# Performance work log

Measured on AMD Instinct MI355X. Metric: run time of the kernel, lower is better.

Reference implementation:

```python
import jax, jax.numpy as jnp
import numpy as np

N = 50000      # nodes
E = 800000     # edges (avg degree 16)
NF = 128       # input feature dim
H = 128        # hidden dim
GAMMA = 1.0    # gm init arg
COS_EPS = 1e-8 # F.cosine_similarity eps
EW_MIN = 1e-4  # edge-weight clamp


def setup_inputs() -> dict:
    key = jax.random.key(0)
    ks = jax.random.split(key, 9)
    x = jax.random.normal(ks[0], (N, NF), dtype=jnp.float32)
    edge_index = jax.random.randint(ks[1], (2, E), 0, N, dtype=jnp.int64)
    sensitive_attr = jax.random.randint(ks[2], (N,), 0, 2, dtype=jnp.int64)
    s1 = 1.0 / np.sqrt(NF)
    s2 = 1.0 / np.sqrt(H)
    W1 = jax.random.normal(ks[3], (NF, H), dtype=jnp.float32) * s1
    b1 = jnp.zeros((H,), dtype=jnp.float32)
    W2 = jax.random.normal(ks[4], (H, H), dtype=jnp.float32) * s2
    b2 = jnp.zeros((H,), dtype=jnp.float32)
    Wc = jax.random.normal(ks[5], (H, 1), dtype=jnp.float32) * s2
    bc = jnp.zeros((1,), dtype=jnp.float32)
    return {"x": x, "edge_index": edge_index, "sensitive_attr": sensitive_attr,
            "W1": W1, "b1": b1, "W2": W2, "b2": b2, "Wc": Wc, "bc": bc}


def gcn_conv(x, W, b, src, dst, ew, n):
    """PyG GCNConv: lin -> symmetric-normalized edge-weighted aggregation (+self loops) -> bias."""
    xt = x @ W                                              # [N,H]
    deg = jax.ops.segment_sum(ew, dst, num_segments=n) + 1.0  # self-loop weight 1
    dinv = jnp.where(deg > 0, deg ** -0.5, 0.0)             # [N]
    norm = dinv[src] * ew * dinv[dst]                       # [E]
    agg = jax.ops.segment_sum(xt[src] * norm[:, None], dst, num_segments=n)
    # self-loop contribution: norm_ii = dinv[i] * 1 * dinv[i]
    return agg + xt * (dinv * dinv)[:, None] + b


def reference(x, edge_index, sensitive_attr, W1, b1, W2, b2, Wc, bc):
    src, dst = edge_index[0], edge_index[1]
    # cosine-similarity edge weights (gather-heavy)
    xs, xd = x[src], x[dst]                                  # [E,F] each
    dot = jnp.sum(xs * xd, axis=1)
    ns = jnp.maximum(jnp.sqrt(jnp.sum(xs * xs, axis=1)), COS_EPS)
    nd = jnp.maximum(jnp.sqrt(jnp.sum(xd * xd, axis=1)), COS_EPS)
    sim = dot / (ns * nd)
    sen_diff = (sensitive_attr[src] != sensitive_attr[dst]).astype(x.dtype)
    ew = jnp.maximum(sim * jnp.exp(-GAMMA * sen_diff), EW_MIN)
    # two GCN layers (dropout is identity in eval mode)
    h = jax.nn.relu(gcn_conv(x, W1, b1, src, dst, ew, N))
    h = jax.nn.relu(gcn_conv(h, W2, b2, src, dst, ew, N))
    y = h @ Wc + bc                                          # [N,1]
    return (y, h)
```

## Files before the change

kernel.cpp:

```cpp
#include <hip/hip_runtime.h>


typedef unsigned short u16;
typedef unsigned int u32;
typedef __attribute__((ext_vector_type(8))) short short8;
typedef __attribute__((ext_vector_type(4))) float floatx4;

__device__ __forceinline__ float bflo(u32 u){ return __uint_as_float(u << 16); }
__device__ __forceinline__ float bfhi(u32 u){ return __uint_as_float(u & 0xFFFF0000u); }
__device__ __forceinline__ float bf1(u16 u){ return __uint_as_float(((u32)u) << 16); }
__device__ __forceinline__ u16 f2bf(float f){
    u32 u = __float_as_uint(f);
    u += 0x7FFFu + ((u >> 16) & 1u);
    return (u16)(u >> 16);
}
__device__ __forceinline__ u32 pack2(float a, float b){
    return (u32)f2bf(a) | ((u32)f2bf(b) << 16);
}
__device__ __forceinline__ float wsum(float v){
#pragma unroll
    for (int o = 32; o > 0; o >>= 1) v += __shfl_xor(v, o, 64);
    return v;
}
__device__ __forceinline__ float ld1(const void* p, size_t idx, int f32){
    return f32 ? ((const float*)p)[idx] : bf1(((const u16*)p)[idx]);
}
__device__ __forceinline__ int ldidx(const int* p, size_t i, int i64){
    return i64 ? p[2 * i] : p[i];
}

__global__ void classify_k(const u32* __restrict__ xw, const int* __restrict__ eiw,
                           int* __restrict__ flags)
{
    __shared__ int c_out, c_nz;
    int t = threadIdx.x;
    if (t == 0) { c_out = 0; c_nz = 0; }
    __syncthreads();
    u32 w = xw[t];
    int e = (w >> 7) & 0xFF;
    int outl = (e < 110 || e > 140) ? 1 : 0;
    int nz = (eiw[2 * t + 1] != 0) ? 1 : 0;
    atomicAdd(&c_out, outl);
    atomicAdd(&c_nz, nz);
    __syncthreads();
    if (t == 0) { flags[0] = (c_out > 256); flags[1] = (c_nz < 256); }
}

__global__ __launch_bounds__(256) void convhist_k(const void* __restrict__ x,
                                                  u32* __restrict__ xb,
                                                  float* __restrict__ rn, int N,
                                                  const int* __restrict__ ei,
                                                  const int* __restrict__ sa,
                                                  int* __restrict__ cnt, int E,
                                                  const void* __restrict__ W1,
                                                  const void* __restrict__ W2,
                                                  uint4* __restrict__ wf1,
                                                  uint4* __restrict__ wf2,
                                                  const int* __restrict__ flags,
                                                  int nbN, int nbE)
{
    int b = blockIdx.x;
    if (b < nbN) {
        int i = b * 4 + (threadIdx.x >> 6);
        if (i >= N) return;
        int lane = threadIdx.x & 63;
        u32 u;
        if (flags[0]) {
            const float* q = (const float*)x + (size_t)i * 128 + lane * 2;
            u = pack2(q[0], q[1]);
        } else u = ((const u32*)x)[(size_t)i * 64 + lane];
        xb[(size_t)i * 64 + lane] = u;
        float f0 = bflo(u), f1 = bfhi(u);
        float ss = wsum(f0 * f0 + f1 * f1);
        if (lane == 0) {
            float r = 1.0f / fmaxf(sqrtf(ss), 1e-8f);
            int a = flags[1] ? sa[2 * (size_t)i] : sa[i];
            rn[i] = a ? -r : r;
        }
    } else if (b < nbN + nbE) {
        int e = (b - nbN) * 256 + threadIdx.x;
        if (e >= E) return;
        int d = ldidx(ei, (size_t)E + e, flags[1]);
        if ((u32)d >= (u32)N) d = 0;
        atomicAdd(&cnt[d], 1);
    } else {
        int slot = (b - nbN - nbE) * 256 + threadIdx.x;
        if (slot >= 4096) return;
        int f32w = flags[0];
        const void* W = (slot < 2048) ? W1 : W2;
        uint4* wf = (slot < 2048) ? wf1 : wf2;
        int s = slot & 2047;
        int lane = s & 63, kk = (s >> 6) & 3, ct = s >> 8;
        int q = lane >> 4, n = lane & 15;
        int col = ct * 16 + n, k0 = kk * 32 + q * 8;
        union { u16 us[8]; uint4 u4; } tmp;
#pragma unroll
        for (int j = 0; j < 8; ++j)
            tmp.us[j] = f2bf(ld1(W, (size_t)(k0 + j) * 128 + col, f32w));
        wf[s] = tmp.u4;
    }
}

__global__ __launch_bounds__(256) void scanA_k(int* __restrict__ cnt,
                                               int* __restrict__ rowp,
                                               int* __restrict__ bsum, int N)
{
    __shared__ int wtot[4];
    int t = threadIdx.x, lane = t & 63, w = t >> 6;
    int i0 = blockIdx.x * 1024 + t * 4;
    int v[4];
#pragma unroll
    for (int k = 0; k < 4; ++k) {
        int i = i0 + k;
        v[k] = (i < N) ? cnt[i] : 0;
        if (i < N) cnt[i] = 0;
    }
    int t4 = v[0] + v[1] + v[2] + v[3];
    int sc = t4;
#pragma unroll
    for (int o = 1; o < 64; o <<= 1) {
        int nv = __shfl_up(sc, o);
        if (lane >= o) sc += nv;
    }
    if (lane == 63) wtot[w] = sc;
    __syncthreads();
    int wo = 0, tot = 0;
#pragma unroll
    for (int k = 0; k < 4; ++k) { int s = wtot[k]; if (k < w) wo += s; tot += s; }
    int pre = wo + sc - t4;
#pragma unroll
    for (int k = 0; k < 4; ++k) {
        int i = i0 + k;
        if (i < N) rowp[i] = pre;
        pre += v[k];
    }
    if (t == 0) bsum[blockIdx.x] = tot;
}

__global__ void scanB_k(int* __restrict__ bsum, int* __restrict__ rowp,
                        int nb, int N)
{
    int lane = threadIdx.x;
    int carry = 0;
    for (int base = 0; base < nb; base += 64) {
        int i = base + lane;
        int v = (i < nb) ? bsum[i] : 0;
        int sc = v;
#pragma unroll
        for (int o = 1; o < 64; o <<= 1) {
            int nv = __shfl_up(sc, o);
            if (lane >= o) sc += nv;
        }
        if (i < nb) bsum[i] = carry + sc - v;
        carry += __shfl(sc, 63);
    }
    if (lane == 0) rowp[N] = carry;
}

__global__ __launch_bounds__(256) void scanC_k(int* __restrict__ rowp,
                                               const int* __restrict__ bsum,
                                               int* __restrict__ bcur, int N)
{
    int off = bsum[blockIdx.x];
    int i0 = blockIdx.x * 1024 + threadIdx.x * 4;
#pragma unroll
    for (int k = 0; k < 4; ++k) {
        int i = i0 + k;
        if (i < N) {
            int v = rowp[i] + off;
            rowp[i] = v;
            if ((i & 255) == 0) bcur[i >> 8] = v;
        }
    }
}

__global__ __launch_bounds__(256) void bucket_k(const int* __restrict__ ei,
                                                int* __restrict__ bcur,
                                                u32* __restrict__ tmp,
                                                int E, int N,
                                                const int* __restrict__ flags)
{
    __shared__ int lh[256];
    __shared__ int gb[256];
    int t = threadIdx.x;
    lh[t] = 0;
    __syncthreads();
    int i64 = flags[1];
    size_t base = (size_t)blockIdx.x * 4096;
    u32 pay[16], meta[16];
#pragma unroll
    for (int k = 0; k < 16; ++k) {
        size_t e = base + (size_t)k * 256 + t;
        if (e < (size_t)E) {
            int s = ldidx(ei, e, i64);
            int d = ldidx(ei, (size_t)E + e, i64);
            if ((u32)s >= (u32)N) s = 0;
            if ((u32)d >= (u32)N) d = 0;
            int b = d >> 8;
            pay[k] = ((u32)s << 8) | ((u32)d & 0xFFu);
            int r = atomicAdd(&lh[b], 1);
            meta[k] = ((u32)r << 8) | (u32)b;
        } else meta[k] = 0xFFFFFFFFu;
    }
    __syncthreads();
    int c = lh[t];
    gb[t] = c ? atomicAdd(&bcur[t], c) : 0;
    __syncthreads();
#pragma unroll
    for (int k = 0; k < 16; ++k) {
        if (meta[k] != 0xFFFFFFFFu) {
            int b = (int)(meta[k] & 0xFFu);
            int r = (int)(meta[k] >> 8);
            tmp[gb[b] + r] = pay[k];
        }
    }
}

__global__ __launch_bounds__(256) void scat2_k(const int* __restrict__ rowp,
                                               int* __restrict__ cnt,
                                               const u32* __restrict__ tmp,
                                               u32* __restrict__ rec,
                                               int N, int E)
{
    int b = blockIdx.x, t = threadIdx.x;
    int n0 = b << 8;
    int n1 = n0 + 256; if (n1 > N) n1 = N;
    int p0 = rowp[n0], p1 = rowp[n1];
    if (p0 < 0) p0 = 0;
    if (p1 > E) p1 = E;
    for (int idx = p0 + t; idx < p1; idx += 256) {
        u32 pay = tmp[idx];
        int d = n0 | (int)(pay & 0xFFu);
        if (d >= N) d = N - 1;
        int s = (int)(pay >> 8);
        int pos = rowp[d] + atomicAdd(&cnt[d], 1);
        if ((u32)pos >= (u32)E) pos = 0;
        rec[pos] = (u32)s;
    }
}

__global__ __launch_bounds__(256) void ewcsr_k(const u32* __restrict__ xb,
                                               const float* __restrict__ rn,
                                               const int* __restrict__ rowp,
                                               u32* __restrict__ rec,
                                               float* __restrict__ dv,
                                               int N, int E)
{
    int i = blockIdx.x * 4 + (threadIdx.x >> 6);
    if (i >= N) return;
    int lane = threadIdx.x & 63, g = lane >> 4, j = lane & 15;
    uint4 D = ((const uint4*)(xb + (size_t)i * 64))[j];
    float rni = rn[i];
    int p0 = rowp[i], p1 = rowp[i + 1];
    if (p0 < 0) p0 = 0;
    if (p1 > E) p1 = E;
    float acc = 0.0f;
    int p = p0 + g;
    for (; p + 4 < p1; p += 8) {
        int s0 = (int)rec[p];     if ((u32)s0 >= (u32)N) s0 = 0;
        int s1 = (int)rec[p + 4]; if ((u32)s1 >= (u32)N) s1 = 0;
        uint4 A0 = ((const uint4*)(xb + (size_t)s0 * 64))[j];
        uint4 A1 = ((const uint4*)(xb + (size_t)s1 * 64))[j];
        float d0 = bflo(A0.x) * bflo(D.x) + bfhi(A0.x) * bfhi(D.x)
                 + bflo(A0.y) * bflo(D.y) + bfhi(A0.y) * bfhi(D.y)
                 + bflo(A0.z) * bflo(D.z) + bfhi(A0.z) * bfhi(D.z)
                 + bflo(A0.w) * bflo(D.w) + bfhi(A0.w) * bfhi(D.w);
        float d1 = bflo(A1.x) * bflo(D.x) + bfhi(A1.x) * bfhi(D.x)
                 + bflo(A1.y) * bflo(D.y) + bfhi(A1.y) * bfhi(D.y)
                 + bflo(A1.z) * bflo(D.z) + bfhi(A1.z) * bfhi(D.z)
                 + bflo(A1.w) * bflo(D.w) + bfhi(A1.w) * bfhi(D.w);
#pragma unroll
        for (int o = 8; o > 0; o >>= 1) {
            d0 += __shfl_xor(d0, o);
            d1 += __shfl_xor(d1, o);
        }
        if (j == 0) {
            float pr0 = rn[s0] * rni;
            float w0 = fmaxf(d0 * fabsf(pr0) *
                             ((pr0 < 0.0f) ? 0.36787944117144233f : 1.0f), 1e-4f);
            u16 wb0 = f2bf(w0);
            rec[p] = ((u32)s0 << 16) | wb0;
            acc += bf1(wb0);
            float pr1 = rn[s1] * rni;
            float w1 = fmaxf(d1 * fabsf(pr1) *
                             ((pr1 < 0.0f) ? 0.36787944117144233f : 1.0f), 1e-4f);
            u16 wb1 = f2bf(w1);
            rec[p + 4] = ((u32)s1 << 16) | wb1;
            acc += bf1(wb1);
        }
    }
    if (p < p1) {
        int s0 = (int)rec[p]; if ((u32)s0 >= (u32)N) s0 = 0;
        uint4 A0 = ((const uint4*)(xb + (size_t)s0 * 64))[j];
        float d0 = bflo(A0.x) * bflo(D.x) + bfhi(A0.x) * bfhi(D.x)
                 + bflo(A0.y) * bflo(D.y) + bfhi(A0.y) * bfhi(D.y)
                 + bflo(A0.z) * bflo(D.z) + bfhi(A0.z) * bfhi(D.z)
                 + bflo(A0.w) * bflo(D.w) + bfhi(A0.w) * bfhi(D.w);
#pragma unroll
        for (int o = 8; o > 0; o >>= 1) d0 += __shfl_xor(d0, o);
        if (j == 0) {
            float pr0 = rn[s0] * rni;
            float w0 = fmaxf(d0 * fabsf(pr0) *
                             ((pr0 < 0.0f) ? 0.36787944117144233f : 1.0f), 1e-4f);
            u16 wb0 = f2bf(w0);
            rec[p] = ((u32)s0 << 16) | wb0;
            acc += bf1(wb0);
        }
    }
    acc += __shfl_xor(acc, 16);
    acc += __shfl_xor(acc, 32);
    if (lane == 0) dv[i] = 1.0f / sqrtf(1.0f + acc);
}

__global__ __launch_bounds__(256) void agg_k(const u32* __restrict__ feat,
                                             const int* __restrict__ rowp,
                                             const u32* __restrict__ rec,
                                             const float* __restrict__ dinv,
                                             u32* __restrict__ Tb, int N, int E)
{
    int i = blockIdx.x * 4 + (threadIdx.x >> 6);
    if (i >= N) return;
    int lane = threadIdx.x & 63;
    float di = dinv[i], sc = di * di;
    u32 u = feat[(size_t)i * 64 + lane];
    float a0 = bflo(u) * sc, a1 = bfhi(u) * sc;
    int p0 = rowp[i], p1 = rowp[i + 1];
    if (p0 < 0) p0 = 0;
    if (p1 > E) p1 = E;
    int p = p0;
    for (; p + 7 < p1; p += 8) {
        u32 r[8]; int s[8]; u32 v[8];
#pragma unroll
        for (int k = 0; k < 8; ++k) {
            r[k] = rec[p + k];
            s[k] = r[k] >> 16;
            if (s[k] >= N) s[k] = 0;
        }
#pragma unroll
        for (int k = 0; k < 8; ++k) v[k] = feat[(size_t)s[k] * 64 + lane];
#pragma unroll
        for (int k = 0; k < 8; ++k) {
            float w = bf1((u16)r[k]) * di * dinv[s[k]];
            a0 = fmaf(w, bflo(v[k]), a0);
            a1 = fmaf(w, bfhi(v[k]), a1);
        }
    }
    for (; p + 1 < p1; p += 2) {
        u32 r0 = rec[p], r1 = rec[p + 1];
        int s0 = r0 >> 16, s1 = r1 >> 16;
        if (s0 >= N) s0 = 0;
        if (s1 >= N) s1 = 0;
        u32 v0 = feat[(size_t)s0 * 64 + lane];
        u32 v1 = feat[(size_t)s1 * 64 + lane];
        float w0 = bf1((u16)r0) * di * dinv[s0];
        float w1 = bf1((u16)r1) * di * dinv[s1];
        a0 = fmaf(w0, bflo(v0), a0); a1 = fmaf(w0, bfhi(v0), a1);
        a0 = fmaf(w1, bflo(v1), a0); a1 = fmaf(w1, bfhi(v1), a1);
    }
    if (p < p1) {
        u32 r0 = rec[p];
        int s0 = r0 >> 16;
        if (s0 >= N) s0 = 0;
        u32 v0 = feat[(size_t)s0 * 64 + lane];
        float w0 = bf1((u16)r0) * di * dinv[s0];
        a0 = fmaf(w0, bflo(v0), a0); a1 = fmaf(w0, bfhi(v0), a1);
    }
    Tb[(size_t)i * 64 + lane] = pack2(a0, a1);
}

__global__ __launch_bounds__(256) void gemm_m(const u32* __restrict__ Tb,
                                              const uint4* __restrict__ wfrag,
                                              const void* __restrict__ bias,
                                              void* __restrict__ out, int outbf,
                                              int N,
                                              const void* __restrict__ Wc,
                                              const void* __restrict__ bc,
                                              float* __restrict__ yout,
                                              const int* __restrict__ flags)
{
    int t = threadIdx.x, wave = t >> 6, lane = t & 63;
    int q = lane >> 4, n = lane & 15;
    int f32w = flags[0];
    int rowbase = blockIdx.x * 64 + wave * 16;
    int arow = rowbase + n; if (arow > N - 1) arow = N - 1;
    const uint4* ap = (const uint4*)(Tb + (size_t)arow * 64);
    short8 a[4];
#pragma unroll
    for (int kk = 0; kk < 4; ++kk) {
        uint4 av = ap[kk * 4 + q];
        a[kk] = *(short8*)&av;
    }
    floatx4 acc[8];
#pragma unroll
    for (int ct = 0; ct < 8; ++ct) acc[ct] = (floatx4){0.f, 0.f, 0.f, 0.f};
#pragma unroll
    for (int ct = 0; ct < 8; ++ct) {
#pragma unroll
        for (int kk = 0; kk < 4; ++kk) {
            uint4 bv = wfrag[(ct * 4 + kk) * 64 + lane];
            acc[ct] = __builtin_amdgcn_mfma_f32_16x16x32_bf16(
                a[kk], *(short8*)&bv, acc[ct], 0, 0, 0);
        }
    }
    float bcv = 0.0f;
    float part[4] = {0.f, 0.f, 0.f, 0.f};
    if (yout) bcv = ld1(bc, 0, f32w);
#pragma unroll
    for (int ct = 0; ct < 8; ++ct) {
        int col = ct * 16 + n;
        float bia = ld1(bias, col, f32w);
        float wcv = yout ? ld1(Wc, col, f32w) : 0.0f;
#pragma unroll
        for (int r = 0; r < 4; ++r) {
            int row = rowbase + q * 4 + r;
            float h = fmaxf(acc[ct][r] + bia, 0.0f);
            if (row < N) {
                if (outbf) ((u16*)out)[(size_t)row * 128 + col] = f2bf(h);
                else       ((float*)out)[(size_t)row * 128 + col] = h;
            }
            part[r] = fmaf(h, wcv, part[r]);
        }
    }
    if (yout) {
#pragma unroll
        for (int r = 0; r < 4; ++r) {
            float pr = part[r];
#pragma unroll
            for (int o = 8; o > 0; o >>= 1) pr += __shfl_xor(pr, o);
            int row = rowbase + q * 4 + r;
            if (n == 0 && row < N) yout[row] = pr + bcv;
        }
    }
}

extern "C" void kernel_launch(void* const* d_in, const int* in_sizes, int n_in,
                              void* d_out, int out_size, void* d_ws, size_t ws_size,
                              hipStream_t stream)
{
    const void* x  = d_in[0];
    const int* ei  = (const int*)d_in[1];
    const int* sa  = (const int*)d_in[2];
    const void* W1 = d_in[3];
    const void* b1 = d_in[4];
    const void* W2 = d_in[5];
    const void* b2 = d_in[6];
    const void* Wc = d_in[7];
    const void* bc = d_in[8];
    const int N = in_sizes[2];
    const int E = in_sizes[1] / 2;

    float* y_out = (float*)d_out;
    float* h_out = y_out + N;
    u32*   Tbuf  = (u32*)d_in[0];
    u32*   tmp   = (u32*)d_in[0];

    const int nbN = (N + 3) / 4, nbE = (E + 255) / 256;
    const int nbS = (N + 1023) / 1024;
    const int NB  = (N + 255) / 256;

    char* p = (char*)d_ws;
    auto carve = [&](size_t bytes) { char* r = p; p += (bytes + 255) & ~(size_t)255; return r; };
    int*   flags = (int*)carve(256);
    float* rn    = (float*)carve((size_t)N * 4);
    float* dinv  = (float*)carve((size_t)N * 4);
    int*   cnt   = (int*)carve((size_t)N * 4);
    int*   rowp  = (int*)carve((size_t)(N + 1) * 4);
    int*   bsum  = (int*)carve((size_t)nbS * 4);
    int*   bcur  = (int*)carve(256 * 4);
    uint4* wf1   = (uint4*)carve(2048 * 16);
    uint4* wf2   = (uint4*)carve(2048 * 16);
    u32*   rec   = (u32*)carve((size_t)E * 4);
    u32*   xb    = (u32*)carve((size_t)N * 64 * 4);

    classify_k<<<1, 1024, 0, stream>>>((const u32*)x, ei, flags);
    hipMemsetAsync(cnt, 0, (size_t)N * 4, stream);
    convhist_k<<<nbN + nbE + 16, 256, 0, stream>>>(x, xb, rn, N, ei, sa, cnt, E,
                                                   W1, W2, wf1, wf2, flags,
                                                   nbN, nbE);
    scanA_k<<<nbS, 256, 0, stream>>>(cnt, rowp, bsum, N);
    scanB_k<<<1, 64, 0, stream>>>(bsum, rowp, nbS, N);
    scanC_k<<<nbS, 256, 0, stream>>>(rowp, bsum, bcur, N);
    bucket_k<<<(E + 4095) / 4096, 256, 0, stream>>>(ei, bcur, tmp, E, N, flags);
    scat2_k<<<NB, 256, 0, stream>>>(rowp, cnt, tmp, rec, N, E);
    ewcsr_k<<<(N + 3) / 4, 256, 0, stream>>>(xb, rn, rowp, rec, dinv, N, E);

    agg_k<<<(N + 3) / 4, 256, 0, stream>>>(xb, rowp, rec, dinv, Tbuf, N, E);
    gemm_m<<<(N + 63) / 64, 256, 0, stream>>>(Tbuf, wf1, b1, xb, 1, N,
                                              nullptr, nullptr, nullptr, flags);
    agg_k<<<(N + 3) / 4, 256, 0, stream>>>(xb, rowp, rec, dinv, Tbuf, N, E);
    gemm_m<<<(N + 63) / 64, 256, 0, stream>>>(Tbuf, wf2, b2, h_out, 0, N,
                                              Wc, bc, y_out, flags);
}
```

Measured before the change: 317.3 us.

## Replace per-node degree histogram and 3-pass scan with bucket histogram and local scan

Instead of a global per-node atomic degree histogram followed by a three-kernel prefix scan, edges are counted per 256-node bucket with shared-memory atomics, then scanned by a single small kernel. Each scatter block builds its own per-node counts and prefix sum in shared memory to produce row pointers and positions within its bucket. This removes a memset, two scan kernels and the global per-node atomics. In exchange the scatter kernel reads its bucket's payloads twice and hardcodes 256 buckets, which assumes N is at most 65536.

```diff
diff --git a/kernel.cpp b/kernel.cpp
--- a/kernel.cpp
+++ b/kernel.cpp
@@ -30,11 +30,12 @@
 }
 
 __global__ void classify_k(const u32* __restrict__ xw, const int* __restrict__ eiw,
-                           int* __restrict__ flags)
+                           int* __restrict__ flags, int* __restrict__ bcnt)
 {
     __shared__ int c_out, c_nz;
     int t = threadIdx.x;
     if (t == 0) { c_out = 0; c_nz = 0; }
+    if (t < 256) bcnt[t] = 0;
     __syncthreads();
     u32 w = xw[t];
     int e = (w >> 7) & 0xFF;
@@ -51,14 +52,15 @@
                                                   float* __restrict__ rn, int N,
                                                   const int* __restrict__ ei,
                                                   const int* __restrict__ sa,
-                                                  int* __restrict__ cnt, int E,
+                                                  int* __restrict__ bcnt, int E,
                                                   const void* __restrict__ W1,
                                                   const void* __restrict__ W2,
                                                   uint4* __restrict__ wf1,
                                                   uint4* __restrict__ wf2,
                                                   const int* __restrict__ flags,
-                                                  int nbN, int nbE)
-{
+                                                  int nbN, int nbH)
+{
+    __shared__ int lb[256];
     int b = blockIdx.x;
     if (b < nbN) {
         int i = b * 4 + (threadIdx.x >> 6);
@@ -77,14 +79,26 @@
             int a = flags[1] ? sa[2 * (size_t)i] : sa[i];
             rn[i] = a ? -r : r;
         }
-    } else if (b < nbN + nbE) {
-        int e = (b - nbN) * 256 + threadIdx.x;
-        if (e >= E) return;
-        int d = ldidx(ei, (size_t)E + e, flags[1]);
-        if ((u32)d >= (u32)N) d = 0;
-        atomicAdd(&cnt[d], 1);
+    } else if (b < nbN + nbH) {
+        int t = threadIdx.x;
+        lb[t] = 0;
+        __syncthreads();
+        int i64 = flags[1];
+        size_t base = (size_t)(b - nbN) * 8192;
+#pragma unroll 4
+        for (int k = 0; k < 32; ++k) {
+            size_t e = base + (size_t)k * 256 + t;
+            if (e < (size_t)E) {
+                int d = ldidx(ei, (size_t)E + e, i64);
+                if ((u32)d >= (u32)N) d = 0;
+                atomicAdd(&lb[d >> 8], 1);
+            }
+        }
+        __syncthreads();
+        int c = lb[t];
+        if (c) atomicAdd(&bcnt[t], c);
     } else {
-        int slot = (b - nbN - nbE) * 256 + threadIdx.x;
+        int slot = (b - nbN - nbH) * 256 + threadIdx.x;
         if (slot >= 4096) return;
         int f32w = flags[0];
         const void* W = (slot < 2048) ? W1 : W2;
@@ -101,77 +115,26 @@
     }
 }
 
-__global__ __launch_bounds__(256) void scanA_k(int* __restrict__ cnt,
-                                               int* __restrict__ rowp,
-                                               int* __restrict__ bsum, int N)
-{
-    __shared__ int wtot[4];
-    int t = threadIdx.x, lane = t & 63, w = t >> 6;
-    int i0 = blockIdx.x * 1024 + t * 4;
-    int v[4];
-#pragma unroll
-    for (int k = 0; k < 4; ++k) {
-        int i = i0 + k;
-        v[k] = (i < N) ? cnt[i] : 0;
-        if (i < N) cnt[i] = 0;
-    }
-    int t4 = v[0] + v[1] + v[2] + v[3];
-    int sc = t4;
-#pragma unroll
-    for (int o = 1; o < 64; o <<= 1) {
-        int nv = __shfl_up(sc, o);
-        if (lane >= o) sc += nv;
-    }
-    if (lane == 63) wtot[w] = sc;
-    __syncthreads();
-    int wo = 0, tot = 0;
-#pragma unroll
-    for (int k = 0; k < 4; ++k) { int s = wtot[k]; if (k < w) wo += s; tot += s; }
-    int pre = wo + sc - t4;
-#pragma unroll
-    for (int k = 0; k < 4; ++k) {
-        int i = i0 + k;
-        if (i < N) rowp[i] = pre;
-        pre += v[k];
-    }
-    if (t == 0) bsum[blockIdx.x] = tot;
-}
-
-__global__ void scanB_k(int* __restrict__ bsum, int* __restrict__ rowp,
-                        int nb, int N)
+__global__ void bscan_k(const int* __restrict__ bcnt, int* __restrict__ bbase,
+                        int* __restrict__ bcur, int* __restrict__ rowp, int N)
 {
     int lane = threadIdx.x;
     int carry = 0;
-    for (int base = 0; base < nb; base += 64) {
+    for (int base = 0; base < 256; base += 64) {
         int i = base + lane;
-        int v = (i < nb) ? bsum[i] : 0;
+        int v = bcnt[i];
         int sc = v;
 #pragma unroll
         for (int o = 1; o < 64; o <<= 1) {
             int nv = __shfl_up(sc, o);
             if (lane >= o) sc += nv;
         }
-        if (i < nb) bsum[i] = carry + sc - v;
+        int excl = carry + sc - v;
+        bbase[i] = excl;
+        bcur[i] = excl;
         carry += __shfl(sc, 63);
     }
-    if (lane == 0) rowp[N] = carry;
-}
-
-__global__ __launch_bounds__(256) void scanC_k(int* __restrict__ rowp,
-                                               const int* __restrict__ bsum,
-                                               int* __restrict__ bcur, int N)
-{
-    int off = bsum[blockIdx.x];
-    int i0 = blockIdx.x * 1024 + threadIdx.x * 4;
-#pragma unroll
-    for (int k = 0; k < 4; ++k) {
-        int i = i0 + k;
-        if (i < N) {
-            int v = rowp[i] + off;
-            rowp[i] = v;
-            if ((i & 255) == 0) bcur[i >> 8] = v;
-        }
-    }
+    if (lane == 0) { bbase[256] = carry; rowp[N] = carry; }
 }
 
 __global__ __launch_bounds__(256) void bucket_k(const int* __restrict__ ei,
@@ -216,26 +179,48 @@
     }
 }
 
-__global__ __launch_bounds__(256) void scat2_k(const int* __restrict__ rowp,
-                                               int* __restrict__ cnt,
+__global__ __launch_bounds__(256) void scat2_k(const int* __restrict__ bbase,
+                                               int* __restrict__ rowp,
                                                const u32* __restrict__ tmp,
                                                u32* __restrict__ rec,
                                                int N, int E)
 {
+    __shared__ int lcnt[256];
+    __shared__ int wtot[4];
     int b = blockIdx.x, t = threadIdx.x;
+    int lane = t & 63, w = t >> 6;
     int n0 = b << 8;
-    int n1 = n0 + 256; if (n1 > N) n1 = N;
-    int p0 = rowp[n0], p1 = rowp[n1];
+    int p0 = bbase[b], p1 = bbase[b + 1];
     if (p0 < 0) p0 = 0;
     if (p1 > E) p1 = E;
+    lcnt[t] = 0;
+    __syncthreads();
+    for (int idx = p0 + t; idx < p1; idx += 256)
+        atomicAdd(&lcnt[tmp[idx] & 0xFFu], 1);
+    __syncthreads();
+    int v = lcnt[t];
+    int sc = v;
+#pragma unroll
+    for (int o = 1; o < 64; o <<= 1) {
+        int nv = __shfl_up(sc, o);
+        if (lane >= o) sc += nv;
+    }
+    if (lane == 63) wtot[w] = sc;
+    __syncthreads();
+    int wo = 0;
+#pragma unroll
+    for (int k = 0; k < 4; ++k) { int s = wtot[k]; if (k < w) wo += s; }
+    int excl = wo + sc - v;
+    int node = n0 + t;
+    if (node < N) rowp[node] = p0 + excl;
+    lcnt[t] = excl;
+    __syncthreads();
     for (int idx = p0 + t; idx < p1; idx += 256) {
         u32 pay = tmp[idx];
-        int d = n0 | (int)(pay & 0xFFu);
-        if (d >= N) d = N - 1;
-        int s = (int)(pay >> 8);
-        int pos = rowp[d] + atomicAdd(&cnt[d], 1);
+        int r = atomicAdd(&lcnt[pay & 0xFFu], 1);
+        int pos = p0 + r;
         if ((u32)pos >= (u32)E) pos = 0;
-        rec[pos] = (u32)s;
+        rec[pos] = pay >> 8;
     }
 }
 
@@ -454,8 +439,8 @@
     u32*   Tbuf  = (u32*)d_in[0];
     u32*   tmp   = (u32*)d_in[0];
 
-    const int nbN = (N + 3) / 4, nbE = (E + 255) / 256;
-    const int nbS = (N + 1023) / 1024;
+    const int nbN = (N + 3) / 4;
+    const int nbH = (E + 8191) / 8192;
     const int NB  = (N + 255) / 256;
 
     char* p = (char*)d_ws;
@@ -463,25 +448,22 @@
     int*   flags = (int*)carve(256);
     float* rn    = (float*)carve((size_t)N * 4);
     float* dinv  = (float*)carve((size_t)N * 4);
-    int*   cnt   = (int*)carve((size_t)N * 4);
     int*   rowp  = (int*)carve((size_t)(N + 1) * 4);
-    int*   bsum  = (int*)carve((size_t)nbS * 4);
+    int*   bcnt  = (int*)carve(256 * 4);
+    int*   bbase = (int*)carve(260 * 4);
     int*   bcur  = (int*)carve(256 * 4);
     uint4* wf1   = (uint4*)carve(2048 * 16);
     uint4* wf2   = (uint4*)carve(2048 * 16);
     u32*   rec   = (u32*)carve((size_t)E * 4);
     u32*   xb    = (u32*)carve((size_t)N * 64 * 4);
 
-    classify_k<<<1, 1024, 0, stream>>>((const u32*)x, ei, flags);
-    hipMemsetAsync(cnt, 0, (size_t)N * 4, stream);
-    convhist_k<<<nbN + nbE + 16, 256, 0, stream>>>(x, xb, rn, N, ei, sa, cnt, E,
+    classify_k<<<1, 1024, 0, stream>>>((const u32*)x, ei, flags, bcnt);
+    convhist_k<<<nbN + nbH + 16, 256, 0, stream>>>(x, xb, rn, N, ei, sa, bcnt, E,
                                                    W1, W2, wf1, wf2, flags,
-                                                   nbN, nbE);
-    scanA_k<<<nbS, 256, 0, stream>>>(cnt, rowp, bsum, N);
-    scanB_k<<<1, 64, 0, stream>>>(bsum, rowp, nbS, N);
-    scanC_k<<<nbS, 256, 0, stream>>>(rowp, bsum, bcur, N);
+                                                   nbN, nbH);
+    bscan_k<<<1, 64, 0, stream>>>(bcnt, bbase, bcur, rowp, N);
     bucket_k<<<(E + 4095) / 4096, 256, 0, stream>>>(ei, bcur, tmp, E, N, flags);
-    scat2_k<<<NB, 256, 0, stream>>>(rowp, cnt, tmp, rec, N, E);
+    scat2_k<<<NB, 256, 0, stream>>>(bbase, rowp, tmp, rec, N, E);
     ewcsr_k<<<(N + 3) / 4, 256, 0, stream>>>(xb, rn, rowp, rec, dinv, N, E);
 
     agg_k<<<(N + 3) / 4, 256, 0, stream>>>(xb, rowp, rec, dinv, Tbuf, N, E);
```

After: 276.0 us. -13.0%, faster.
